# Optimization experiments

Hardware: AMD Instinct MI355X
Metric: run time of the kernel (lower is better)

The kernel has to match this reference:

```python
import jax, jax.numpy as jnp
import numpy as np

B, S, D_MODEL, H, D_K, D_V = 2, 2048, 1024, 16, 64, 64


def setup_inputs() -> dict:
    key = jax.random.key(0)
    ks = jax.random.split(key, 12)
    s = 0.02
    inp = {
        "Q": jax.random.normal(ks[0], (B, S, D_MODEL), jnp.float32),
        "K": jax.random.normal(ks[1], (B, S, D_MODEL), jnp.float32),
        "V": jax.random.normal(ks[2], (B, S, D_MODEL), jnp.float32),
        # causal 0/1 mask, broadcastable to [B, H, S, S]
        "mask": jnp.tril(jnp.ones((S, S), jnp.int32))[None, None, :, :],
        "Wq": jax.random.normal(ks[3], (D_MODEL, H * D_K), jnp.float32) * s,
        "bq": jnp.zeros((H * D_K,), jnp.float32),
        "Wk": jax.random.normal(ks[4], (D_MODEL, H * D_K), jnp.float32) * s,
        "bk": jnp.zeros((H * D_K,), jnp.float32),
        "Wv": jax.random.normal(ks[5], (D_MODEL, H * D_V), jnp.float32) * s,
        "bv": jnp.zeros((H * D_V,), jnp.float32),
        "Wo": jax.random.normal(ks[6], (H * D_V, D_MODEL), jnp.float32) * s,
        "bo": jnp.zeros((D_MODEL,), jnp.float32),
    }
    return inp


def reference(Q, K, V, mask, Wq, bq, Wk, bk, Wv, bv, Wo, bo):
    b = Q.shape[0]
    # project and split heads: [B, S, H*dk] -> [B, H, S, dk]
    q = (Q @ Wq + bq).reshape(b, -1, H, D_K).transpose(0, 2, 1, 3)
    k = (K @ Wk + bk).reshape(b, -1, H, D_K).transpose(0, 2, 1, 3)
    v = (V @ Wv + bv).reshape(b, -1, H, D_V).transpose(0, 2, 1, 3)
    scale = 1.0 / np.sqrt(D_K).astype(np.float32)
    scores = jnp.einsum("bhqd,bhkd->bhqk", q, k) * scale
    scores = jnp.where(mask == 0, jnp.float32(-1e9), scores)
    attn = jax.nn.softmax(scores, axis=-1)
    context = jnp.einsum("bhqk,bhkd->bhqd", attn, v)
    context = context.transpose(0, 2, 1, 3).reshape(b, -1, H * D_V)
    output = context @ Wo + bo  # dropout is identity in eval
    return output, attn
```

## Files before the change

kernel.cpp:

```cpp
#include <hip/hip_runtime.h>
#include <math.h>

#define S_LEN 2048
#define DMODEL 1024
#define NHEAD 16
#define HD 64
#define NBATCH 2

using short8  = __attribute__((ext_vector_type(8))) short;
using ushort8 = __attribute__((ext_vector_type(8))) unsigned short;
using floatx4 = __attribute__((ext_vector_type(4))) float;

__device__ __forceinline__ unsigned short f2b(float f) {
    unsigned int u = __float_as_uint(f);
    unsigned int r = (u + 0x7FFFu + ((u >> 16) & 1u)) >> 16;
    return (unsigned short)r;
}

__device__ __forceinline__ void gll16(const void* g, void* l) {
    __builtin_amdgcn_global_load_lds(
        (const __attribute__((address_space(1))) unsigned int*)g,
        (__attribute__((address_space(3))) unsigned int*)l, 16, 0, 0);
}

__global__ __launch_bounds__(256)
void convert_bf16(const float* __restrict__ src, unsigned short* __restrict__ dst, int n4)
{
    int i = blockIdx.x * 256 + threadIdx.x;
    if (i < n4) {
        float4 v = ((const float4*)src)[i];
        ushort4 o;
        o.x = f2b(v.x); o.y = f2b(v.y); o.z = f2b(v.z); o.w = f2b(v.w);
        ((ushort4*)dst)[i] = o;
    }
}

__global__ __launch_bounds__(256)
void transpose_w(const float* __restrict__ W0, const float* __restrict__ W1,
                 const float* __restrict__ W2, const float* __restrict__ W3,
                 unsigned short* __restrict__ T0, unsigned short* __restrict__ T1,
                 unsigned short* __restrict__ T2, unsigned short* __restrict__ T3)
{
    __shared__ float t[64][65];
    const float* W; unsigned short* T;
    switch (blockIdx.z) {
        case 0: W = W0; T = T0; break;
        case 1: W = W1; T = T1; break;
        case 2: W = W2; T = T2; break;
        default: W = W3; T = T3; break;
    }
    const int tid = threadIdx.x;
    const int c0 = blockIdx.x * 64;
    const int r0 = blockIdx.y * 64;
    #pragma unroll
    for (int i = 0; i < 4; ++i) {
        int c = tid + i * 256;
        int r = c >> 4, off = (c & 15) * 4;
        float4 v = *(const float4*)(W + (size_t)(r0 + r) * DMODEL + c0 + off);
        t[r][off + 0] = v.x; t[r][off + 1] = v.y;
        t[r][off + 2] = v.z; t[r][off + 3] = v.w;
    }
    __syncthreads();
    #pragma unroll
    for (int i = 0; i < 4; ++i) {
        int c = tid + i * 256;
        int n = c >> 4, off = (c & 15) * 4;
        ushort4 o;
        o.x = f2b(t[off + 0][n]); o.y = f2b(t[off + 1][n]);
        o.z = f2b(t[off + 2][n]); o.w = f2b(t[off + 3][n]);
        *(ushort4*)(T + (size_t)(c0 + n) * DMODEL + r0 + off) = o;
    }
}

__global__ __launch_bounds__(256)
void gemm_qkv(const unsigned short* __restrict__ X0, const unsigned short* __restrict__ X1,
              const unsigned short* __restrict__ X2,
              const unsigned short* __restrict__ W0, const unsigned short* __restrict__ W1,
              const unsigned short* __restrict__ W2,
              const float* __restrict__ b0, const float* __restrict__ b1,
              const float* __restrict__ b2,
              unsigned short* __restrict__ o0, unsigned short* __restrict__ o1,
              unsigned short* __restrict__ o2)
{
    __shared__ unsigned short Xs[128 * 64];
    __shared__ unsigned short Ws[128 * 64];

    const unsigned short* X  = (blockIdx.z == 0) ? X0 : (blockIdx.z == 1) ? X1 : X2;
    const unsigned short* Wt = (blockIdx.z == 0) ? W0 : (blockIdx.z == 1) ? W1 : W2;
    const float* bias        = (blockIdx.z == 0) ? b0 : (blockIdx.z == 1) ? b1 : b2;
    unsigned short* outp     = (blockIdx.z == 0) ? o0 : (blockIdx.z == 1) ? o1 : o2;

    const int tid = threadIdx.x;
    const int lane = tid & 63, w = tid >> 6;
    const int l15 = lane & 15, l4 = lane >> 4;
    const int wr = w >> 1, wc = w & 1;
    const int row0 = blockIdx.y * 128;
    const int col0 = blockIdx.x * 128;

    const int srow = lane >> 3;
    const int sblk = (lane & 7) ^ srow;

    floatx4 acc[4][4] = {};

    for (int k0 = 0; k0 < DMODEL; k0 += 64) {
        __syncthreads();
        #pragma unroll
        for (int i = 0; i < 4; ++i)
            gll16(X + (size_t)(row0 + w * 32 + i * 8 + srow) * DMODEL + k0 + sblk * 8,
                  &Xs[(w * 32 + i * 8) * 64]);
        #pragma unroll
        for (int i = 0; i < 4; ++i)
            gll16(Wt + (size_t)(col0 + w * 32 + i * 8 + srow) * DMODEL + k0 + sblk * 8,
                  &Ws[(w * 32 + i * 8) * 64]);
        asm volatile("s_waitcnt vmcnt(0)" ::: "memory");
        __syncthreads();

        #pragma unroll
        for (int ks = 0; ks < 2; ++ks) {
            short8 a[4], b[4];
            #pragma unroll
            for (int m = 0; m < 4; ++m) {
                const int r = wr * 64 + m * 16 + l15;
                a[m] = *(const short8*)&Xs[r * 64 + (((ks * 4 + l4) ^ (r & 7)) << 3)];
            }
            #pragma unroll
            for (int n = 0; n < 4; ++n) {
                const int r = wc * 64 + n * 16 + l15;
                b[n] = *(const short8*)&Ws[r * 64 + (((ks * 4 + l4) ^ (r & 7)) << 3)];
            }
            #pragma unroll
            for (int m = 0; m < 4; ++m)
                #pragma unroll
                for (int n = 0; n < 4; ++n)
                    acc[m][n] = __builtin_amdgcn_mfma_f32_16x16x32_bf16(
                        a[m], b[n], acc[m][n], 0, 0, 0);
        }
    }

    float bl[4];
    #pragma unroll
    for (int n = 0; n < 4; ++n)
        bl[n] = bias[col0 + wc * 64 + n * 16 + l15];

    #pragma unroll
    for (int m = 0; m < 4; ++m)
        #pragma unroll
        for (int n = 0; n < 4; ++n) {
            const int gc = col0 + wc * 64 + n * 16 + l15;
            const int h = gc >> 6, d = gc & 63;
            #pragma unroll
            for (int reg = 0; reg < 4; ++reg) {
                const int gr = row0 + wr * 64 + m * 16 + l4 * 4 + reg;
                const int bb = gr >> 11, s = gr & 2047;
                outp[(((size_t)bb * NHEAD + h) * S_LEN + s) * HD + d] =
                    f2b(acc[m][n][reg] + bl[n]);
            }
        }
}

__global__ __launch_bounds__(256)
void gemm_out(const unsigned short* __restrict__ X, const unsigned short* __restrict__ Wt,
              const float* __restrict__ bias, float* __restrict__ out)
{
    __shared__ unsigned short Xs[128 * 64];
    __shared__ unsigned short Ws[128 * 64];

    const int tid = threadIdx.x;
    const int lane = tid & 63, w = tid >> 6;
    const int l15 = lane & 15, l4 = lane >> 4;
    const int wr = w >> 1, wc = w & 1;
    const int row0 = blockIdx.y * 128;
    const int col0 = blockIdx.x * 128;

    const int srow = lane >> 3;
    const int sblk = (lane & 7) ^ srow;

    floatx4 acc[4][4] = {};

    for (int k0 = 0; k0 < DMODEL; k0 += 64) {
        __syncthreads();
        #pragma unroll
        for (int i = 0; i < 4; ++i)
            gll16(X + (size_t)(row0 + w * 32 + i * 8 + srow) * DMODEL + k0 + sblk * 8,
                  &Xs[(w * 32 + i * 8) * 64]);
        #pragma unroll
        for (int i = 0; i < 4; ++i)
            gll16(Wt + (size_t)(col0 + w * 32 + i * 8 + srow) * DMODEL + k0 + sblk * 8,
                  &Ws[(w * 32 + i * 8) * 64]);
        asm volatile("s_waitcnt vmcnt(0)" ::: "memory");
        __syncthreads();

        #pragma unroll
        for (int ks = 0; ks < 2; ++ks) {
            short8 a[4], b[4];
            #pragma unroll
            for (int m = 0; m < 4; ++m) {
                const int r = wr * 64 + m * 16 + l15;
                a[m] = *(const short8*)&Xs[r * 64 + (((ks * 4 + l4) ^ (r & 7)) << 3)];
            }
            #pragma unroll
            for (int n = 0; n < 4; ++n) {
                const int r = wc * 64 + n * 16 + l15;
                b[n] = *(const short8*)&Ws[r * 64 + (((ks * 4 + l4) ^ (r & 7)) << 3)];
            }
            #pragma unroll
            for (int m = 0; m < 4; ++m)
                #pragma unroll
                for (int n = 0; n < 4; ++n)
                    acc[m][n] = __builtin_amdgcn_mfma_f32_16x16x32_bf16(
                        a[m], b[n], acc[m][n], 0, 0, 0);
        }
    }

    float bl[4];
    #pragma unroll
    for (int n = 0; n < 4; ++n)
        bl[n] = bias[col0 + wc * 64 + n * 16 + l15];

    #pragma unroll
    for (int m = 0; m < 4; ++m)
        #pragma unroll
        for (int n = 0; n < 4; ++n) {
            const int gc = col0 + wc * 64 + n * 16 + l15;
            #pragma unroll
            for (int reg = 0; reg < 4; ++reg) {
                const int gr = row0 + wr * 64 + m * 16 + l4 * 4 + reg;
                out[(size_t)gr * DMODEL + gc] = acc[m][n][reg] + bl[n];
            }
        }
}

__device__ __forceinline__ int vt_off(int d, int jblk) {
    return d * 64 + ((jblk ^ ((d ^ (d >> 3)) & 7)) << 3);
}

__global__ __launch_bounds__(256)
void attn_mfma(const unsigned short* __restrict__ qg, const unsigned short* __restrict__ kg,
               const unsigned short* __restrict__ vg, float* __restrict__ attn,
               unsigned short* __restrict__ ctx)
{
    __shared__ unsigned short Ks[64 * 64];
    __shared__ unsigned short Vt[64 * 64];
    __shared__ unsigned short Ps[128 * 88];

    const int tid = threadIdx.x;
    const int lane = tid & 63, w = tid >> 6;
    const int l15 = lane & 15, l4 = lane >> 4;

    const int i0 = blockIdx.x;
    const int jmap = (i0 & 7) * 64 + (i0 >> 3);
    const int qx = jmap & 15, bh = jmap >> 4;
    const int qb = (bh < 16) ? qx : 15 - qx;
    const int row0 = qb * 128;

    const int srow = lane >> 3;
    const int sblk = (lane & 7) ^ srow;

    const float C2 = 0.18033688011112042f;

    const unsigned short* qh = qg + (size_t)bh * S_LEN * HD;
    const unsigned short* kh = kg + (size_t)bh * S_LEN * HD;
    const unsigned short* vh = vg + (size_t)bh * S_LEN * HD;
    float* attnh = attn + (size_t)bh * S_LEN * S_LEN;

    short8 qa[2][2];
    #pragma unroll
    for (int m = 0; m < 2; ++m)
        #pragma unroll
        for (int ks = 0; ks < 2; ++ks)
            qa[m][ks] = *(const short8*)(qh + (size_t)(row0 + w * 32 + m * 16 + l15) * HD
                                         + ks * 32 + l4 * 8);

    const int nt = 2 * qb + 2;

    float lsum[2][4] = {};
    for (int jt = 0; jt < nt; ++jt) {
        __syncthreads();
        #pragma unroll
        for (int i = 0; i < 2; ++i)
            gll16(kh + (size_t)(jt * 64 + w * 16 + i * 8 + srow) * HD + sblk * 8,
                  &Ks[(w * 16 + i * 8) * 64]);
        asm volatile("s_waitcnt vmcnt(0)" ::: "memory");
        __syncthreads();

        floatx4 sf[2][4] = {};
        #pragma unroll
        for (int ks = 0; ks < 2; ++ks) {
            short8 kb[4];
            #pragma unroll
            for (int c = 0; c < 4; ++c) {
                const int r = c * 16 + l15;
                kb[c] = *(const short8*)&Ks[r * 64 + (((ks * 4 + l4) ^ (r & 7)) << 3)];
            }
            #pragma unroll
            for (int m = 0; m < 2; ++m)
                #pragma unroll
                for (int c = 0; c < 4; ++c)
                    sf[m][c] = __builtin_amdgcn_mfma_f32_16x16x32_bf16(
                        qa[m][ks], kb[c], sf[m][c], 0, 0, 0);
        }

        #pragma unroll
        for (int m = 0; m < 2; ++m) {
            const int rbase = row0 + w * 32 + m * 16;
            if (jt * 64 + 63 <= rbase) {
                #pragma unroll
                for (int c = 0; c < 4; ++c)
                    #pragma unroll
                    for (int reg = 0; reg < 4; ++reg)
                        lsum[m][reg] += exp2f(sf[m][c][reg] * C2);
            } else {
                #pragma unroll
                for (int c = 0; c < 4; ++c) {
                    const int jcol = jt * 64 + c * 16 + l15;
                    #pragma unroll
                    for (int reg = 0; reg < 4; ++reg) {
                        const int grow = rbase + l4 * 4 + reg;
                        lsum[m][reg] += (jcol <= grow) ? exp2f(sf[m][c][reg] * C2) : 0.f;
                    }
                }
            }
        }
    }

    float nl2[2][4];
    #pragma unroll
    for (int m = 0; m < 2; ++m)
        #pragma unroll
        for (int reg = 0; reg < 4; ++reg) {
            float s = lsum[m][reg];
            #pragma unroll
            for (int off = 1; off < 16; off <<= 1)
                s += __shfl_xor(s, off);
            nl2[m][reg] = -__log2f(s);
        }

    floatx4 o[2][4] = {};
    for (int jt = 0; jt < nt; ++jt) {
        __syncthreads();
        ushort8 vv[2];
        #pragma unroll
        for (int i = 0; i < 2; ++i) {
            const int c = tid + i * 256;
            const int jj = c >> 3, d0 = (c & 7) * 8;
            vv[i] = *(const ushort8*)(vh + (size_t)(jt * 64 + jj) * HD + d0);
        }
        #pragma unroll
        for (int i = 0; i < 2; ++i)
            gll16(kh + (size_t)(jt * 64 + w * 16 + i * 8 + srow) * HD + sblk * 8,
                  &Ks[(w * 16 + i * 8) * 64]);
        #pragma unroll
        for (int i = 0; i < 2; ++i) {
            const int c = tid + i * 256;
            const int jj = c >> 3, d0 = (c & 7) * 8;
            #pragma unroll
            for (int e = 0; e < 8; ++e)
                Vt[vt_off(d0 + e, jj >> 3) + (jj & 7)] = vv[i][e];
        }
        asm volatile("s_waitcnt vmcnt(0)" ::: "memory");
        __syncthreads();

        floatx4 sf[2][4] = {};
        #pragma unroll
        for (int ks = 0; ks < 2; ++ks) {
            short8 kb[4];
            #pragma unroll
            for (int c = 0; c < 4; ++c) {
                const int r = c * 16 + l15;
                kb[c] = *(const short8*)&Ks[r * 64 + (((ks * 4 + l4) ^ (r & 7)) << 3)];
            }
            #pragma unroll
            for (int m = 0; m < 2; ++m)
                #pragma unroll
                for (int c = 0; c < 4; ++c)
                    sf[m][c] = __builtin_amdgcn_mfma_f32_16x16x32_bf16(
                        qa[m][ks], kb[c], sf[m][c], 0, 0, 0);
        }

        #pragma unroll
        for (int m = 0; m < 2; ++m) {
            const int rbase = row0 + w * 32 + m * 16;
            const bool full = (jt * 64 + 63 <= rbase);
            #pragma unroll
            for (int c = 0; c < 4; ++c) {
                const int jcol = jt * 64 + c * 16 + l15;
                #pragma unroll
                for (int reg = 0; reg < 4; ++reg) {
                    const int rl = w * 32 + m * 16 + l4 * 4 + reg;
                    const int grow = row0 + rl;
                    float p = exp2f(fmaf(sf[m][c][reg], C2, nl2[m][reg]));
                    if (!full && jcol > grow) p = 0.f;
                    attnh[(size_t)grow * S_LEN + jcol] = p;
                    Ps[rl * 88 + c * 16 + l15] = f2b(p);
                }
            }
        }
        __syncthreads();

        #pragma unroll
        for (int m = 0; m < 2; ++m)
            #pragma unroll
            for (int ks = 0; ks < 2; ++ks) {
                const short8 pa = *(const short8*)&Ps[(w * 32 + m * 16 + l15) * 88
                                                      + ks * 32 + l4 * 8];
                #pragma unroll
                for (int c = 0; c < 4; ++c) {
                    const short8 vb = *(const short8*)&Vt[vt_off(c * 16 + l15, ks * 4 + l4)];
                    o[m][c] = __builtin_amdgcn_mfma_f32_16x16x32_bf16(pa, vb, o[m][c], 0, 0, 0);
                }
            }
    }

    const int b = bh >> 4, h = bh & 15;
    #pragma unroll
    for (int m = 0; m < 2; ++m)
        #pragma unroll
        for (int c = 0; c < 4; ++c)
            #pragma unroll
            for (int reg = 0; reg < 4; ++reg) {
                const int gr = row0 + w * 32 + m * 16 + l4 * 4 + reg;
                const int d = c * 16 + l15;
                ctx[((size_t)b * S_LEN + gr) * DMODEL + h * HD + d] = f2b(o[m][c][reg]);
            }

    const float4 z4 = {0.f, 0.f, 0.f, 0.f};
    for (int jt = nt; jt < S_LEN / 64; ++jt) {
        #pragma unroll
        for (int i = 0; i < 8; ++i) {
            const int idx = tid + i * 256;
            const int r = idx >> 4, off = (idx & 15) * 4;
            *(float4*)(attnh + (size_t)(row0 + r) * S_LEN + jt * 64 + off) = z4;
        }
    }
}

extern "C" void kernel_launch(void* const* d_in, const int* in_sizes, int n_in,
                              void* d_out, int out_size, void* d_ws, size_t ws_size,
                              hipStream_t stream)
{
    const float* Q  = (const float*)d_in[0];
    const float* K  = (const float*)d_in[1];
    const float* V  = (const float*)d_in[2];
    const float* Wq = (const float*)d_in[4];
    const float* bq = (const float*)d_in[5];
    const float* Wk = (const float*)d_in[6];
    const float* bk = (const float*)d_in[7];
    const float* Wv = (const float*)d_in[8];
    const float* bv = (const float*)d_in[9];
    const float* Wo = (const float*)d_in[10];
    const float* bo = (const float*)d_in[11];

    float* out  = (float*)d_out;
    float* attn = out + (size_t)NBATCH * S_LEN * DMODEL;

    const size_t per = (size_t)NBATCH * S_LEN * DMODEL;
    const size_t wsz = (size_t)DMODEL * DMODEL;
    unsigned short* Xq  = (unsigned short*)d_ws;
    unsigned short* Xk  = Xq + per;
    unsigned short* Xv  = Xk + per;
    unsigned short* Wtq = Xv + per;
    unsigned short* Wtk = Wtq + wsz;
    unsigned short* Wtv = Wtk + wsz;
    unsigned short* Wto = Wtv + wsz;
    unsigned short* qhw = Wto + wsz;
    unsigned short* khw = qhw + per;
    unsigned short* vhw = khw + per;
    unsigned short* ctx = vhw + per;

    const int n4 = (int)(per / 4);
    convert_bf16<<<(n4 + 255) / 256, 256, 0, stream>>>(Q, Xq, n4);
    convert_bf16<<<(n4 + 255) / 256, 256, 0, stream>>>(K, Xk, n4);
    convert_bf16<<<(n4 + 255) / 256, 256, 0, stream>>>(V, Xv, n4);
    transpose_w<<<dim3(16, 16, 4), 256, 0, stream>>>(Wq, Wk, Wv, Wo, Wtq, Wtk, Wtv, Wto);

    gemm_qkv<<<dim3(DMODEL / 128, (NBATCH * S_LEN) / 128, 3), 256, 0, stream>>>(
        Xq, Xk, Xv, Wtq, Wtk, Wtv, bq, bk, bv, qhw, khw, vhw);

    attn_mfma<<<512, 256, 0, stream>>>(qhw, khw, vhw, attn, ctx);

    gemm_out<<<dim3(DMODEL / 128, (NBATCH * S_LEN) / 128), 256, 0, stream>>>(
        ctx, Wto, bo, out);
}
```

Measured before the change: 280.4 us.

## Double-buffer K/V tiles, coalesce attn stores via LDS, add nontemporal stores

Double-buffers the K and V shared-memory tiles so the next tile's global loads are issued before the current tile's MFMA work, which removes one barrier per iteration. The attention-probability output is now written from the bf16 P tile in LDS as coalesced nontemporal float4 stores, replacing scattered per-element fp32 stores. MFMA sections are wrapped in s_setprio. The side effect is that the attn output values are now rounded to bf16 precision, and LDS use doubles for K and V.

```diff
diff --git a/kernel.cpp b/kernel.cpp
--- a/kernel.cpp
+++ b/kernel.cpp
@@ -15,6 +15,9 @@
     unsigned int u = __float_as_uint(f);
     unsigned int r = (u + 0x7FFFu + ((u >> 16) & 1u)) >> 16;
     return (unsigned short)r;
+}
+__device__ __forceinline__ float b2f(unsigned short b) {
+    return __uint_as_float(((unsigned int)b) << 16);
 }
 
 __device__ __forceinline__ void gll16(const void* g, void* l) {
@@ -239,8 +242,8 @@
                const unsigned short* __restrict__ vg, float* __restrict__ attn,
                unsigned short* __restrict__ ctx)
 {
-    __shared__ unsigned short Ks[64 * 64];
-    __shared__ unsigned short Vt[64 * 64];
+    __shared__ unsigned short Ks[2 * 64 * 64];
+    __shared__ unsigned short Vt[2 * 64 * 64];
     __shared__ unsigned short Ps[128 * 88];
 
     const int tid = threadIdx.x;
@@ -273,24 +276,33 @@
 
     const int nt = 2 * qb + 2;
 
+    #pragma unroll
+    for (int i = 0; i < 2; ++i)
+        gll16(kh + (size_t)(w * 16 + i * 8 + srow) * HD + sblk * 8,
+              &Ks[(w * 16 + i * 8) * 64]);
+
     float lsum[2][4] = {};
     for (int jt = 0; jt < nt; ++jt) {
-        __syncthreads();
-        #pragma unroll
-        for (int i = 0; i < 2; ++i)
-            gll16(kh + (size_t)(jt * 64 + w * 16 + i * 8 + srow) * HD + sblk * 8,
-                  &Ks[(w * 16 + i * 8) * 64]);
+        const int cur = jt & 1;
         asm volatile("s_waitcnt vmcnt(0)" ::: "memory");
         __syncthreads();
+        if (jt + 1 < nt) {
+            #pragma unroll
+            for (int i = 0; i < 2; ++i)
+                gll16(kh + (size_t)((jt + 1) * 64 + w * 16 + i * 8 + srow) * HD + sblk * 8,
+                      &Ks[(cur ^ 1) * 4096 + (w * 16 + i * 8) * 64]);
+        }
 
         floatx4 sf[2][4] = {};
+        __builtin_amdgcn_s_setprio(1);
         #pragma unroll
         for (int ks = 0; ks < 2; ++ks) {
             short8 kb[4];
             #pragma unroll
             for (int c = 0; c < 4; ++c) {
                 const int r = c * 16 + l15;
-                kb[c] = *(const short8*)&Ks[r * 64 + (((ks * 4 + l4) ^ (r & 7)) << 3)];
+                kb[c] = *(const short8*)&Ks[cur * 4096 + r * 64
+                                            + (((ks * 4 + l4) ^ (r & 7)) << 3)];
             }
             #pragma unroll
             for (int m = 0; m < 2; ++m)
@@ -299,6 +311,7 @@
                     sf[m][c] = __builtin_amdgcn_mfma_f32_16x16x32_bf16(
                         qa[m][ks], kb[c], sf[m][c], 0, 0, 0);
         }
+        __builtin_amdgcn_s_setprio(0);
 
         #pragma unroll
         for (int m = 0; m < 2; ++m) {
@@ -335,39 +348,43 @@
             nl2[m][reg] = -__log2f(s);
         }
 
+    #pragma unroll
+    for (int i = 0; i < 2; ++i)
+        gll16(kh + (size_t)(w * 16 + i * 8 + srow) * HD + sblk * 8,
+              &Ks[(w * 16 + i * 8) * 64]);
+    const int jj0 = tid >> 3, d0v = (tid & 7) * 8;
+    ushort8 vva = *(const ushort8*)(vh + (size_t)jj0 * HD + d0v);
+    ushort8 vvb = *(const ushort8*)(vh + (size_t)(jj0 + 32) * HD + d0v);
+
     floatx4 o[2][4] = {};
     for (int jt = 0; jt < nt; ++jt) {
-        __syncthreads();
-        ushort8 vv[2];
-        #pragma unroll
-        for (int i = 0; i < 2; ++i) {
-            const int c = tid + i * 256;
-            const int jj = c >> 3, d0 = (c & 7) * 8;
-            vv[i] = *(const ushort8*)(vh + (size_t)(jt * 64 + jj) * HD + d0);
-        }
-        #pragma unroll
-        for (int i = 0; i < 2; ++i)
-            gll16(kh + (size_t)(jt * 64 + w * 16 + i * 8 + srow) * HD + sblk * 8,
-                  &Ks[(w * 16 + i * 8) * 64]);
-        #pragma unroll
-        for (int i = 0; i < 2; ++i) {
-            const int c = tid + i * 256;
-            const int jj = c >> 3, d0 = (c & 7) * 8;
-            #pragma unroll
-            for (int e = 0; e < 8; ++e)
-                Vt[vt_off(d0 + e, jj >> 3) + (jj & 7)] = vv[i][e];
-        }
+        const int cur = jt & 1;
         asm volatile("s_waitcnt vmcnt(0)" ::: "memory");
         __syncthreads();
+        #pragma unroll
+        for (int e = 0; e < 8; ++e) {
+            Vt[cur * 4096 + vt_off(d0v + e, jj0 >> 3) + (jj0 & 7)] = vva[e];
+            Vt[cur * 4096 + vt_off(d0v + e, (jj0 + 32) >> 3) + ((jj0 + 32) & 7)] = vvb[e];
+        }
+        if (jt + 1 < nt) {
+            #pragma unroll
+            for (int i = 0; i < 2; ++i)
+                gll16(kh + (size_t)((jt + 1) * 64 + w * 16 + i * 8 + srow) * HD + sblk * 8,
+                      &Ks[(cur ^ 1) * 4096 + (w * 16 + i * 8) * 64]);
+            vva = *(const ushort8*)(vh + (size_t)((jt + 1) * 64 + jj0) * HD + d0v);
+            vvb = *(const ushort8*)(vh + (size_t)((jt + 1) * 64 + jj0 + 32) * HD + d0v);
+        }
 
         floatx4 sf[2][4] = {};
+        __builtin_amdgcn_s_setprio(1);
         #pragma unroll
         for (int ks = 0; ks < 2; ++ks) {
             short8 kb[4];
             #pragma unroll
             for (int c = 0; c < 4; ++c) {
                 const int r = c * 16 + l15;
-                kb[c] = *(const short8*)&Ks[r * 64 + (((ks * 4 + l4) ^ (r & 7)) << 3)];
+                kb[c] = *(const short8*)&Ks[cur * 4096 + r * 64
+                                            + (((ks * 4 + l4) ^ (r & 7)) << 3)];
             }
             #pragma unroll
             for (int m = 0; m < 2; ++m)
@@ -376,6 +393,7 @@
                     sf[m][c] = __builtin_amdgcn_mfma_f32_16x16x32_bf16(
                         qa[m][ks], kb[c], sf[m][c], 0, 0, 0);
         }
+        __builtin_amdgcn_s_setprio(0);
 
         #pragma unroll
         for (int m = 0; m < 2; ++m) {
@@ -387,16 +405,26 @@
                 #pragma unroll
                 for (int reg = 0; reg < 4; ++reg) {
                     const int rl = w * 32 + m * 16 + l4 * 4 + reg;
-                    const int grow = row0 + rl;
                     float p = exp2f(fmaf(sf[m][c][reg], C2, nl2[m][reg]));
-                    if (!full && jcol > grow) p = 0.f;
-                    attnh[(size_t)grow * S_LEN + jcol] = p;
+                    if (!full && jcol > rbase + l4 * 4 + reg) p = 0.f;
                     Ps[rl * 88 + c * 16 + l15] = f2b(p);
                 }
             }
         }
         __syncthreads();
 
+        #pragma unroll
+        for (int i2 = 0; i2 < 8; ++i2) {
+            const int idx = tid + i2 * 256;
+            const int r = idx >> 4, c4 = (idx & 15) * 4;
+            const ushort4 pb = *(const ushort4*)&Ps[r * 88 + c4];
+            floatx4 pf;
+            pf[0] = b2f(pb.x); pf[1] = b2f(pb.y); pf[2] = b2f(pb.z); pf[3] = b2f(pb.w);
+            __builtin_nontemporal_store(
+                pf, (floatx4*)(attnh + (size_t)(row0 + r) * S_LEN + jt * 64 + c4));
+        }
+
+        __builtin_amdgcn_s_setprio(1);
         #pragma unroll
         for (int m = 0; m < 2; ++m)
             #pragma unroll
@@ -405,10 +433,12 @@
                                                       + ks * 32 + l4 * 8];
                 #pragma unroll
                 for (int c = 0; c < 4; ++c) {
-                    const short8 vb = *(const short8*)&Vt[vt_off(c * 16 + l15, ks * 4 + l4)];
+                    const short8 vb = *(const short8*)&Vt[cur * 4096
+                                                          + vt_off(c * 16 + l15, ks * 4 + l4)];
                     o[m][c] = __builtin_amdgcn_mfma_f32_16x16x32_bf16(pa, vb, o[m][c], 0, 0, 0);
                 }
             }
+        __builtin_amdgcn_s_setprio(0);
     }
 
     const int b = bh >> 4, h = bh & 15;
@@ -423,13 +453,14 @@
                 ctx[((size_t)b * S_LEN + gr) * DMODEL + h * HD + d] = f2b(o[m][c][reg]);
             }
 
-    const float4 z4 = {0.f, 0.f, 0.f, 0.f};
+    const floatx4 z4 = {0.f, 0.f, 0.f, 0.f};
     for (int jt = nt; jt < S_LEN / 64; ++jt) {
         #pragma unroll
         for (int i = 0; i < 8; ++i) {
             const int idx = tid + i * 256;
             const int r = idx >> 4, off = (idx & 15) * 4;
-            *(float4*)(attnh + (size_t)(row0 + r) * S_LEN + jt * 64 + off) = z4;
+            __builtin_nontemporal_store(
+                z4, (floatx4*)(attnh + (size_t)(row0 + r) * S_LEN + jt * 64 + off));
         }
     }
 }
```

After: 298.7 us. 6.6% more time.

## Halve attention query tile to 64 rows, doubling blocks; merge bf16 convert launches

Applied to the files above, without the earlier changes.

The attention kernel now gives each block 64 query rows instead of 128, with one 16-row MFMA tile per wave, and launches 1024 blocks with a new causal-balanced block-to-(head, query-block) mapping. This is meant to improve load balance and occupancy on the many-CU GPU. In exchange, each K/V tile loaded into LDS is reused by half as many query rows. The three fp32-to-bf16 conversion launches are also merged into one launch using blockIdx.z to cut launch overhead.

```diff
diff --git a/kernel.cpp b/kernel.cpp
--- a/kernel.cpp
+++ b/kernel.cpp
@@ -24,8 +24,13 @@
 }
 
 __global__ __launch_bounds__(256)
-void convert_bf16(const float* __restrict__ src, unsigned short* __restrict__ dst, int n4)
-{
+void convert_bf16(const float* __restrict__ S0, const float* __restrict__ S1,
+                  const float* __restrict__ S2,
+                  unsigned short* __restrict__ D0, unsigned short* __restrict__ D1,
+                  unsigned short* __restrict__ D2, int n4)
+{
+    const float* src = (blockIdx.z == 0) ? S0 : (blockIdx.z == 1) ? S1 : S2;
+    unsigned short* dst = (blockIdx.z == 0) ? D0 : (blockIdx.z == 1) ? D1 : D2;
     int i = blockIdx.x * 256 + threadIdx.x;
     if (i < n4) {
         float4 v = ((const float4*)src)[i];
@@ -241,17 +246,18 @@
 {
     __shared__ unsigned short Ks[64 * 64];
     __shared__ unsigned short Vt[64 * 64];
-    __shared__ unsigned short Ps[128 * 88];
+    __shared__ unsigned short Ps[64 * 88];
 
     const int tid = threadIdx.x;
     const int lane = tid & 63, w = tid >> 6;
     const int l15 = lane & 15, l4 = lane >> 4;
 
     const int i0 = blockIdx.x;
-    const int jmap = (i0 & 7) * 64 + (i0 >> 3);
-    const int qx = jmap & 15, bh = jmap >> 4;
-    const int qb = (bh < 16) ? qx : 15 - qx;
-    const int row0 = qb * 128;
+    const int local = i0 >> 3;
+    const int bh = (i0 & 7) * 4 + (local & 3);
+    const int qx = local >> 2;
+    const int qb = (bh & 1) ? (31 - qx) : qx;
+    const int row0 = qb * 64;
 
     const int srow = lane >> 3;
     const int sblk = (lane & 7) ^ srow;
@@ -263,17 +269,14 @@
     const unsigned short* vh = vg + (size_t)bh * S_LEN * HD;
     float* attnh = attn + (size_t)bh * S_LEN * S_LEN;
 
-    short8 qa[2][2];
-    #pragma unroll
-    for (int m = 0; m < 2; ++m)
-        #pragma unroll
-        for (int ks = 0; ks < 2; ++ks)
-            qa[m][ks] = *(const short8*)(qh + (size_t)(row0 + w * 32 + m * 16 + l15) * HD
-                                         + ks * 32 + l4 * 8);
-
-    const int nt = 2 * qb + 2;
-
-    float lsum[2][4] = {};
+    short8 qa[2];
+    #pragma unroll
+    for (int ks = 0; ks < 2; ++ks)
+        qa[ks] = *(const short8*)(qh + (size_t)(row0 + w * 16 + l15) * HD + ks * 32 + l4 * 8);
+
+    const int nt = qb + 1;
+
+    float lsum[4] = {};
     for (int jt = 0; jt < nt; ++jt) {
         __syncthreads();
         #pragma unroll
@@ -283,7 +286,7 @@
         asm volatile("s_waitcnt vmcnt(0)" ::: "memory");
         __syncthreads();
 
-        floatx4 sf[2][4] = {};
+        floatx4 sf[4] = {};
         #pragma unroll
         for (int ks = 0; ks < 2; ++ks) {
             short8 kb[4];
@@ -293,140 +296,113 @@
                 kb[c] = *(const short8*)&Ks[r * 64 + (((ks * 4 + l4) ^ (r & 7)) << 3)];
             }
             #pragma unroll
-            for (int m = 0; m < 2; ++m)
+            for (int c = 0; c < 4; ++c)
+                sf[c] = __builtin_amdgcn_mfma_f32_16x16x32_bf16(qa[ks], kb[c], sf[c], 0, 0, 0);
+        }
+
+        const int rbase = row0 + w * 16;
+        if (jt * 64 + 63 <= rbase) {
+            #pragma unroll
+            for (int c = 0; c < 4; ++c)
                 #pragma unroll
-                for (int c = 0; c < 4; ++c)
-                    sf[m][c] = __builtin_amdgcn_mfma_f32_16x16x32_bf16(
-                        qa[m][ks], kb[c], sf[m][c], 0, 0, 0);
-        }
-
-        #pragma unroll
-        for (int m = 0; m < 2; ++m) {
-            const int rbase = row0 + w * 32 + m * 16;
-            if (jt * 64 + 63 <= rbase) {
-                #pragma unroll
-                for (int c = 0; c < 4; ++c)
-                    #pragma unroll
-                    for (int reg = 0; reg < 4; ++reg)
-                        lsum[m][reg] += exp2f(sf[m][c][reg] * C2);
-            } else {
-                #pragma unroll
-                for (int c = 0; c < 4; ++c) {
-                    const int jcol = jt * 64 + c * 16 + l15;
-                    #pragma unroll
-                    for (int reg = 0; reg < 4; ++reg) {
-                        const int grow = rbase + l4 * 4 + reg;
-                        lsum[m][reg] += (jcol <= grow) ? exp2f(sf[m][c][reg] * C2) : 0.f;
-                    }
-                }
-            }
-        }
-    }
-
-    float nl2[2][4];
-    #pragma unroll
-    for (int m = 0; m < 2; ++m)
-        #pragma unroll
-        for (int reg = 0; reg < 4; ++reg) {
-            float s = lsum[m][reg];
-            #pragma unroll
-            for (int off = 1; off < 16; off <<= 1)
-                s += __shfl_xor(s, off);
-            nl2[m][reg] = -__log2f(s);
-        }
-
-    floatx4 o[2][4] = {};
-    for (int jt = 0; jt < nt; ++jt) {
-        __syncthreads();
-        ushort8 vv[2];
-        #pragma unroll
-        for (int i = 0; i < 2; ++i) {
-            const int c = tid + i * 256;
-            const int jj = c >> 3, d0 = (c & 7) * 8;
-            vv[i] = *(const ushort8*)(vh + (size_t)(jt * 64 + jj) * HD + d0);
-        }
-        #pragma unroll
-        for (int i = 0; i < 2; ++i)
-            gll16(kh + (size_t)(jt * 64 + w * 16 + i * 8 + srow) * HD + sblk * 8,
-                  &Ks[(w * 16 + i * 8) * 64]);
-        #pragma unroll
-        for (int i = 0; i < 2; ++i) {
-            const int c = tid + i * 256;
-            const int jj = c >> 3, d0 = (c & 7) * 8;
-            #pragma unroll
-            for (int e = 0; e < 8; ++e)
-                Vt[vt_off(d0 + e, jj >> 3) + (jj & 7)] = vv[i][e];
-        }
-        asm volatile("s_waitcnt vmcnt(0)" ::: "memory");
-        __syncthreads();
-
-        floatx4 sf[2][4] = {};
-        #pragma unroll
-        for (int ks = 0; ks < 2; ++ks) {
-            short8 kb[4];
-            #pragma unroll
-            for (int c = 0; c < 4; ++c) {
-                const int r = c * 16 + l15;
-                kb[c] = *(const short8*)&Ks[r * 64 + (((ks * 4 + l4) ^ (r & 7)) << 3)];
-            }
-            #pragma unroll
-            for (int m = 0; m < 2; ++m)
-                #pragma unroll
-                for (int c = 0; c < 4; ++c)
-                    sf[m][c] = __builtin_amdgcn_mfma_f32_16x16x32_bf16(
-                        qa[m][ks], kb[c], sf[m][c], 0, 0, 0);
-        }
-
-        #pragma unroll
-        for (int m = 0; m < 2; ++m) {
-            const int rbase = row0 + w * 32 + m * 16;
-            const bool full = (jt * 64 + 63 <= rbase);
+                for (int reg = 0; reg < 4; ++reg)
+                    lsum[reg] += exp2f(sf[c][reg] * C2);
+        } else {
             #pragma unroll
             for (int c = 0; c < 4; ++c) {
                 const int jcol = jt * 64 + c * 16 + l15;
                 #pragma unroll
                 for (int reg = 0; reg < 4; ++reg) {
-                    const int rl = w * 32 + m * 16 + l4 * 4 + reg;
-                    const int grow = row0 + rl;
-                    float p = exp2f(fmaf(sf[m][c][reg], C2, nl2[m][reg]));
-                    if (!full && jcol > grow) p = 0.f;
-                    attnh[(size_t)grow * S_LEN + jcol] = p;
-                    Ps[rl * 88 + c * 16 + l15] = f2b(p);
+                    const int grow = rbase + l4 * 4 + reg;
+                    lsum[reg] += (jcol <= grow) ? exp2f(sf[c][reg] * C2) : 0.f;
                 }
             }
         }
-        __syncthreads();
-
-        #pragma unroll
-        for (int m = 0; m < 2; ++m)
-            #pragma unroll
-            for (int ks = 0; ks < 2; ++ks) {
-                const short8 pa = *(const short8*)&Ps[(w * 32 + m * 16 + l15) * 88
-                                                      + ks * 32 + l4 * 8];
-                #pragma unroll
-                for (int c = 0; c < 4; ++c) {
-                    const short8 vb = *(const short8*)&Vt[vt_off(c * 16 + l15, ks * 4 + l4)];
-                    o[m][c] = __builtin_amdgcn_mfma_f32_16x16x32_bf16(pa, vb, o[m][c], 0, 0, 0);
-                }
-            }
+    }
+
+    float nl2[4];
+    #pragma unroll
+    for (int reg = 0; reg < 4; ++reg) {
+        float s = lsum[reg];
+        #pragma unroll
+        for (int off = 1; off < 16; off <<= 1)
+            s += __shfl_xor(s, off);
+        nl2[reg] = -__log2f(s);
+    }
+
+    floatx4 o[4] = {};
+    for (int jt = 0; jt < nt; ++jt) {
+        __syncthreads();
+        const int jj0 = tid >> 3, d0v = (tid & 7) * 8;
+        ushort8 vva = *(const ushort8*)(vh + (size_t)(jt * 64 + jj0) * HD + d0v);
+        ushort8 vvb = *(const ushort8*)(vh + (size_t)(jt * 64 + jj0 + 32) * HD + d0v);
+        #pragma unroll
+        for (int i = 0; i < 2; ++i)
+            gll16(kh + (size_t)(jt * 64 + w * 16 + i * 8 + srow) * HD + sblk * 8,
+                  &Ks[(w * 16 + i * 8) * 64]);
+        #pragma unroll
+        for (int e = 0; e < 8; ++e) {
+            Vt[vt_off(d0v + e, jj0 >> 3) + (jj0 & 7)] = vva[e];
+            Vt[vt_off(d0v + e, (jj0 + 32) >> 3) + ((jj0 + 32) & 7)] = vvb[e];
+        }
+        asm volatile("s_waitcnt vmcnt(0)" ::: "memory");
+        __syncthreads();
+
+        floatx4 sf[4] = {};
+        #pragma unroll
+        for (int ks = 0; ks < 2; ++ks) {
+            short8 kb[4];
+            #pragma unroll
+            for (int c = 0; c < 4; ++c) {
+                const int r = c * 16 + l15;
+                kb[c] = *(const short8*)&Ks[r * 64 + (((ks * 4 + l4) ^ (r & 7)) << 3)];
+            }
+            #pragma unroll
+            for (int c = 0; c < 4; ++c)
+                sf[c] = __builtin_amdgcn_mfma_f32_16x16x32_bf16(qa[ks], kb[c], sf[c], 0, 0, 0);
+        }
+
+        const int rbase = row0 + w * 16;
+        const bool full = (jt * 64 + 63 <= rbase);
+        #pragma unroll
+        for (int c = 0; c < 4; ++c) {
+            const int jcol = jt * 64 + c * 16 + l15;
+            #pragma unroll
+            for (int reg = 0; reg < 4; ++reg) {
+                const int rl = w * 16 + l4 * 4 + reg;
+                float p = exp2f(fmaf(sf[c][reg], C2, nl2[reg]));
+                if (!full && jcol > rbase + l4 * 4 + reg) p = 0.f;
+                attnh[(size_t)(row0 + rl) * S_LEN + jcol] = p;
+                Ps[rl * 88 + c * 16 + l15] = f2b(p);
+            }
+        }
+        __syncthreads();
+
+        #pragma unroll
+        for (int ks = 0; ks < 2; ++ks) {
+            const short8 pa = *(const short8*)&Ps[(w * 16 + l15) * 88 + ks * 32 + l4 * 8];
+            #pragma unroll
+            for (int c = 0; c < 4; ++c) {
+                const short8 vb = *(const short8*)&Vt[vt_off(c * 16 + l15, ks * 4 + l4)];
+                o[c] = __builtin_amdgcn_mfma_f32_16x16x32_bf16(pa, vb, o[c], 0, 0, 0);
+            }
+        }
     }
 
     const int b = bh >> 4, h = bh & 15;
     #pragma unroll
-    for (int m = 0; m < 2; ++m)
-        #pragma unroll
-        for (int c = 0; c < 4; ++c)
-            #pragma unroll
-            for (int reg = 0; reg < 4; ++reg) {
-                const int gr = row0 + w * 32 + m * 16 + l4 * 4 + reg;
-                const int d = c * 16 + l15;
-                ctx[((size_t)b * S_LEN + gr) * DMODEL + h * HD + d] = f2b(o[m][c][reg]);
-            }
+    for (int c = 0; c < 4; ++c)
+        #pragma unroll
+        for (int reg = 0; reg < 4; ++reg) {
+            const int gr = row0 + w * 16 + l4 * 4 + reg;
+            const int d = c * 16 + l15;
+            ctx[((size_t)b * S_LEN + gr) * DMODEL + h * HD + d] = f2b(o[c][reg]);
+        }
 
     const float4 z4 = {0.f, 0.f, 0.f, 0.f};
     for (int jt = nt; jt < S_LEN / 64; ++jt) {
         #pragma unroll
-        for (int i = 0; i < 8; ++i) {
+        for (int i = 0; i < 4; ++i) {
             const int idx = tid + i * 256;
             const int r = idx >> 4, off = (idx & 15) * 4;
             *(float4*)(attnh + (size_t)(row0 + r) * S_LEN + jt * 64 + off) = z4;
@@ -468,15 +444,14 @@
     unsigned short* ctx = vhw + per;
 
     const int n4 = (int)(per / 4);
-    convert_bf16<<<(n4 + 255) / 256, 256, 0, stream>>>(Q, Xq, n4);
-    convert_bf16<<<(n4 + 255) / 256, 256, 0, stream>>>(K, Xk, n4);
-    convert_bf16<<<(n4 + 255) / 256, 256, 0, stream>>>(V, Xv, n4);
+    convert_bf16<<<dim3((n4 + 255) / 256, 1, 3), 256, 0, stream>>>(
+        Q, K, V, Xq, Xk, Xv, n4);
     transpose_w<<<dim3(16, 16, 4), 256, 0, stream>>>(Wq, Wk, Wv, Wo, Wtq, Wtk, Wtv, Wto);
 
     gemm_qkv<<<dim3(DMODEL / 128, (NBATCH * S_LEN) / 128, 3), 256, 0, stream>>>(
         Xq, Xk, Xv, Wtq, Wtk, Wtv, bq, bk, bv, qhw, khw, vhw);
 
-    attn_mfma<<<512, 256, 0, stream>>>(qhw, khw, vhw, attn, ctx);
+    attn_mfma<<<1024, 256, 0, stream>>>(qhw, khw, vhw, attn, ctx);
 
     gemm_out<<<dim3(DMODEL / 128, (NBATCH * S_LEN) / 128), 256, 0, stream>>>(
         ctx, Wto, bo, out);
```

After: 278.5 us. About the same (-0.7%).
